# Optimization experiments

Measured on AMD Instinct MI355X. Metric: run time of the kernel, lower is better.

The kernel has to match this reference:

```python
import jax, jax.numpy as jnp
import numpy as np
from jax import lax

B, CIN, COUT, H, W = 4, 256, 256, 64, 64
K, DG, STRIDE, PAD, DIL = 3, 1, 1, 1, 1
K2 = K * K
CG = CIN // DG
HO = (H + 2 * PAD - DIL * (K - 1) - 1) // STRIDE + 1
WO = (W + 2 * PAD - DIL * (K - 1) - 1) // STRIDE + 1


def setup_inputs() -> dict:
    key = jax.random.key(0)
    k1, k2, k3 = jax.random.split(key, 3)
    inputs = jax.random.normal(k1, (B, CIN, H, W), jnp.float32)
    # original init_offset() zeros these; small random weights instead so offsets ~0.5px
    w_off = jax.random.normal(k2, (3 * DG * K2, CIN, K, K), jnp.float32) * 0.01
    b_off = jnp.zeros((3 * DG * K2,), jnp.float32)
    w_dcn = jax.random.normal(k3, (COUT, CIN, K, K), jnp.float32) * (1.0 / np.sqrt(CIN * K2))
    b_dcn = jnp.zeros((COUT,), jnp.float32)
    return {"inputs": inputs, "w_off": w_off, "b_off": b_off, "w_dcn": w_dcn, "b_dcn": b_dcn}


def _conv2d(x, w, b):
    y = lax.conv_general_dilated(x, w, (STRIDE, STRIDE), [(PAD, PAD), (PAD, PAD)],
                                 rhs_dilation=(DIL, DIL),
                                 dimension_numbers=("NCHW", "OIHW", "NCHW"))
    return y + b[None, :, None, None]


def _dcn_forward(inputs, w_off, b_off, w_dcn, b_dcn):
    # offset/mask branch (standard conv), then chunk into o1, o2, mask
    om = _conv2d(inputs, w_off, b_off)                      # [B, 3*DG*K2, HO, WO]
    o1, o2, m = jnp.split(om, 3, axis=1)
    offset = jnp.concatenate([o1, o2], axis=1)              # [B, 2*DG*K2, HO, WO]
    mask = jax.nn.sigmoid(m)                                # [B, DG*K2, HO, WO]

    # DCNv2 offset layout: per deformable group, K2 taps of (dy, dx)
    off = offset.reshape(B, DG, K2, 2, HO, WO)
    dy, dx = off[:, :, :, 0], off[:, :, :, 1]               # [B, DG, K2, HO, WO]

    taps = jnp.arange(K2)
    ki = (taps // K).astype(jnp.float32)
    kj = (taps % K).astype(jnp.float32)
    hb = (jnp.arange(HO, dtype=jnp.float32) * STRIDE - PAD)
    wb = (jnp.arange(WO, dtype=jnp.float32) * STRIDE - PAD)
    py = dy + hb[None, None, None, :, None] + (ki * DIL)[None, None, :, None, None]
    px = dx + wb[None, None, None, None, :] + (kj * DIL)[None, None, :, None, None]

    y0f, x0f = jnp.floor(py), jnp.floor(px)
    ly, lx = py - y0f, px - x0f
    y0, x0 = y0f.astype(jnp.int32), x0f.astype(jnp.int32)
    y1, x1 = y0 + 1, x0 + 1

    flat = inputs.reshape(B, DG, CG, H * W)

    def corner(yi, xi, wgt):
        valid = (yi >= 0) & (yi < H) & (xi >= 0) & (xi < W)
        yc = jnp.clip(yi, 0, H - 1)
        xc = jnp.clip(xi, 0, W - 1)
        idx = (yc * W + xc).reshape(B, DG, 1, K2 * HO * WO)
        idx = jnp.broadcast_to(idx, (B, DG, CG, K2 * HO * WO))
        v = jnp.take_along_axis(flat, idx, axis=3).reshape(B, DG, CG, K2, HO, WO)
        w = jnp.where(valid, wgt, 0.0)[:, :, None]          # zero outside (zero-pad bilinear)
        return v * w

    val = (corner(y0, x0, (1 - ly) * (1 - lx)) + corner(y0, x1, (1 - ly) * lx)
           + corner(y1, x0, ly * (1 - lx)) + corner(y1, x1, ly * lx))

    cols = val * mask.reshape(B, DG, 1, K2, HO, WO)         # modulated columns
    cols = cols.reshape(B, CIN * K2, HO * WO)
    out = jnp.einsum("ok,bkn->bon", w_dcn.reshape(COUT, CIN * K2), cols)
    out = out + b_dcn[None, :, None]
    return out.reshape(B, COUT, HO, WO)


def reference(inputs, w_off, b_off, w_dcn, b_dcn):
    return _dcn_forward(inputs, w_off, b_off, w_dcn, b_dcn)
```

## Files before the change

### kernel.cpp

```cpp
#include <hip/hip_runtime.h>
#include <hip/hip_bf16.h>

typedef __bf16 bf16x8 __attribute__((ext_vector_type(8)));
typedef __bf16 bf16x4 __attribute__((ext_vector_type(4)));
typedef float f32x4 __attribute__((ext_vector_type(4)));
typedef unsigned int u32x4 __attribute__((ext_vector_type(4)));

#define CIN 256
#define COUT 256
#define KDIM 2304

__device__ __forceinline__ void gload_lds16(const void* g, void* l) {
  __builtin_amdgcn_global_load_lds(
      (__attribute__((address_space(1))) unsigned int*)g,
      (__attribute__((address_space(3))) unsigned int*)l, 16, 0, 0);
}

__global__ __launch_bounds__(256) void k_prep_all(const float* __restrict__ wdcn,
                                                  const float* __restrict__ woff,
                                                  __bf16* __restrict__ Ag,
                                                  __bf16* __restrict__ Ah,
                                                  __bf16* __restrict__ Al) {
  int bid = blockIdx.x, tid = threadIdx.x;
  if (bid < 2304) {
    int t = bid * 256 + tid;
    int cout = t / KDIM;
    int r = t - cout * KDIM;
    int tap = r >> 8, cin = r & 255;
    Ag[t] = (__bf16)wdcn[(cout * 256 + cin) * 9 + tap];
  } else {
    int t = (bid - 2304) * 256 + tid;
    int j = t & 7;
    int l = (t >> 3) & 63;
    int mh = (t >> 9) & 1;
    int s = t >> 10;
    int tap = s >> 3, cc = s & 7;
    int ki = tap / 3, kj = tap - ki * 3;
    int oc = mh * 16 + (l & 15);
    int cin = cc * 32 + ((l >> 4) << 3) + j;
    float v = (oc < 27) ? woff[((oc * 256 + cin) * 3 + ki) * 3 + kj] : 0.f;
    __bf16 hi = (__bf16)v;
    __bf16 lo = (__bf16)(v - (float)hi);
    Ah[t] = hi;
    Al[t] = lo;
  }
}

__global__ __launch_bounds__(256) void k_tr(const float* __restrict__ in,
                                            __bf16* __restrict__ inT) {
  int h = blockIdx.x, b = blockIdx.y;
  int c = threadIdx.x;
  const float* src = in + ((((b << 8) + c) << 6) + h) * 64;
  __bf16* dst = inT + (((b << 12) + (h << 6)) << 8) + c;
#pragma unroll
  for (int w4 = 0; w4 < 16; ++w4) {
    f32x4 v = *(const f32x4*)(src + (w4 << 2));
#pragma unroll
    for (int k = 0; k < 4; ++k) dst[(((w4 << 2) + k)) << 8] = (__bf16)v[k];
  }
}

__global__ __launch_bounds__(256) void k_conv(const __bf16* __restrict__ inT,
                                              const __bf16* __restrict__ Ah,
                                              const __bf16* __restrict__ Al,
                                              float* __restrict__ omp) {
  __shared__ __bf16 xh[3 * 4 * 66 * 8];
  int tid = threadIdx.x;
  int l = tid & 63, wn = tid >> 6;
  int ho = blockIdx.x, b = blockIdx.y, ct = blockIdx.z;

  f32x4 acc[2];
  acc[0] = (f32x4){0.f, 0.f, 0.f, 0.f};
  acc[1] = (f32x4){0.f, 0.f, 0.f, 0.f};

  for (int chunk = 0; chunk < 4; ++chunk) {
    int cin0 = ct * 128 + chunk * 32;
    for (int i = tid; i < 792; i += 256) {
      int c = i % 66;
      int t2 = i / 66;
      int u = t2 & 3, r = t2 >> 2;
      int h = ho - 1 + r, w = c - 1;
      bool ok = ((unsigned)h < 64u) & ((unsigned)w < 64u);
      bf16x8 hv = (bf16x8){};
      if (ok)
        hv = *(const bf16x8*)(inT + ((((b << 12) + (h << 6) + w)) << 8) + cin0 +
                              (u << 3));
      *(bf16x8*)&xh[((r * 4 + u) * 66 + c) << 3] = hv;
    }
    __syncthreads();
    int scc = ct * 4 + chunk;
#pragma unroll
    for (int tap = 0; tap < 9; ++tap) {
      int s = tap * 8 + scc;
      int ki = tap / 3, kj = tap - ki * 3;
      bf16x8 ah0 = *(const bf16x8*)(Ah + (((s * 2 + 0) * 64 + l) << 3));
      bf16x8 ah1 = *(const bf16x8*)(Ah + (((s * 2 + 1) * 64 + l) << 3));
      bf16x8 al0 = *(const bf16x8*)(Al + (((s * 2 + 0) * 64 + l) << 3));
      bf16x8 al1 = *(const bf16x8*)(Al + (((s * 2 + 1) * 64 + l) << 3));
      int u = l >> 4;
      int sc = (wn << 4) + (l & 15) + kj;
      bf16x8 bh = *(const bf16x8*)&xh[((ki * 4 + u) * 66 + sc) << 3];
      acc[0] = __builtin_amdgcn_mfma_f32_16x16x32_bf16(ah0, bh, acc[0], 0, 0, 0);
      acc[1] = __builtin_amdgcn_mfma_f32_16x16x32_bf16(ah1, bh, acc[1], 0, 0, 0);
      acc[0] = __builtin_amdgcn_mfma_f32_16x16x32_bf16(al0, bh, acc[0], 0, 0, 0);
      acc[1] = __builtin_amdgcn_mfma_f32_16x16x32_bf16(al1, bh, acc[1], 0, 0, 0);
    }
    __syncthreads();
  }
  int n = (ho << 6) + (wn << 4) + (l & 15);
#pragma unroll
  for (int mh = 0; mh < 2; ++mh)
#pragma unroll
    for (int r = 0; r < 4; ++r) {
      int oc = mh * 16 + ((l >> 4) << 2) + r;
      if (oc < 27)
        omp[(((ct * 4 + b) * 27 + oc) << 12) + n] = acc[mh][r];
    }
}

__global__ __launch_bounds__(512, 4) void k_gemm(const __bf16* __restrict__ inT,
                                                 const float* __restrict__ omp,
                                                 const float* __restrict__ boff,
                                                 const __bf16* __restrict__ Ag,
                                                 const float* __restrict__ bdcn,
                                                 float* __restrict__ out) {
  __shared__ u32x4 sA[2048];
  __shared__ u32x4 sB[256];
  int tid = threadIdx.x;
  int l = tid & 63;
  int w = tid >> 6;
  int wm = w & 3, wh = w >> 2;
  int id = blockIdx.x;
  int x = id & 7, t = id >> 3;
  int b = x >> 1;
  int ntile = ((x & 1) << 6) + t;
  int sn = tid >> 4;
  int sc = tid & 15;
  int n_g = (ntile << 5) + sn;
  const __bf16* tb = inT + ((b << 12) << 8);

  f32x4 acc[4];
#pragma unroll
  for (int i = 0; i < 4; ++i) acc[i] = (f32x4){0.f, 0.f, 0.f, 0.f};

  float w00 = 0.f, w01 = 0.f, w10 = 0.f, w11 = 0.f;
  int o00 = 0, o01 = 0, o10 = 0, o11 = 0;

  for (int step = 0; step < 36; ++step) {
    int tap = step >> 2;
    int cin0 = (step & 3) << 6;
    if ((step & 3) == 0) {
      int ki = tap / 3, kj = tap - ki * 3;
      float dy = omp[((b * 27 + 2 * tap) << 12) + n_g] +
                 omp[(((4 + b) * 27 + 2 * tap) << 12) + n_g] + boff[2 * tap];
      float dx = omp[((b * 27 + 2 * tap + 1) << 12) + n_g] +
                 omp[(((4 + b) * 27 + 2 * tap + 1) << 12) + n_g] + boff[2 * tap + 1];
      float mv = omp[((b * 27 + 18 + tap) << 12) + n_g] +
                 omp[(((4 + b) * 27 + 18 + tap) << 12) + n_g] + boff[18 + tap];
      float msk = 1.f / (1.f + __expf(-mv));
      float py = dy + (float)((n_g >> 6) - 1 + ki);
      float px = dx + (float)((n_g & 63) - 1 + kj);
      float y0f = floorf(py), x0f = floorf(px);
      float ly = py - y0f, lx = px - x0f;
      int y0 = (int)y0f, x0 = (int)x0f;
      int y1 = y0 + 1, x1 = x0 + 1;
      bool vy0 = (y0 >= 0) & (y0 < 64), vy1 = (y1 >= 0) & (y1 < 64);
      bool vx0 = (x0 >= 0) & (x0 < 64), vx1 = (x1 >= 0) & (x1 < 64);
      float hy = 1.f - ly, hx = 1.f - lx;
      w00 = (vy0 & vx0) ? hy * hx * msk : 0.f;
      w01 = (vy0 & vx1) ? hy * lx * msk : 0.f;
      w10 = (vy1 & vx0) ? ly * hx * msk : 0.f;
      w11 = (vy1 & vx1) ? ly * lx * msk : 0.f;
      int y0c = min(max(y0, 0), 63), y1c = min(max(y1, 0), 63);
      int x0c = min(max(x0, 0), 63), x1c = min(max(x1, 0), 63);
      o00 = (y0c << 6) + x0c;
      o01 = (y0c << 6) + x1c;
      o10 = (y1c << 6) + x0c;
      o11 = (y1c << 6) + x1c;
    }
    int cb0 = cin0 + (sc << 2);
    bf16x4 cA = *(const bf16x4*)(tb + (o00 << 8) + cb0);
    bf16x4 cB = *(const bf16x4*)(tb + (o01 << 8) + cb0);
    bf16x4 cC = *(const bf16x4*)(tb + (o10 << 8) + cb0);
    bf16x4 cD = *(const bf16x4*)(tb + (o11 << 8) + cb0);
    bf16x4 vv;
#pragma unroll
    for (int j = 0; j < 4; ++j) {
      vv[j] = (__bf16)(w00 * (float)cA[j] + w01 * (float)cB[j] +
                       w10 * (float)cC[j] + w11 * (float)cD[j]);
    }
    __syncthreads();
    int kk0 = (tap << 8) + cin0;
#pragma unroll
    for (int i = 0; i < 4; ++i) {
      int slot = i * 512 + tid;
      int m = slot >> 3, j = slot & 7;
      int csrc = j ^ (m & 7);
      const __bf16* src = Ag + m * KDIM + kk0 + (csrc << 3);
      gload_lds16((const void*)src, (void*)&sA[i * 512 + (tid & ~63)]);
    }
    {
      unsigned long long* sB64 = (unsigned long long*)sB;
      int slot = (sn << 3) + ((sc >> 1) ^ (sn & 7));
      sB64[slot * 2 + (sc & 1)] = __builtin_bit_cast(unsigned long long, vv);
    }
    __syncthreads();
#pragma unroll
    for (int kt = 0; kt < 2; ++kt) {
      bf16x8 af[4], bfr;
      int cc = (kt << 2) + (l >> 4);
#pragma unroll
      for (int mf = 0; mf < 4; ++mf) {
        int m = (wm << 6) + (mf << 4) + (l & 15);
        af[mf] = __builtin_bit_cast(bf16x8, sA[(m << 3) + (cc ^ (m & 7))]);
      }
      {
        int n = (wh << 4) + (l & 15);
        bfr = __builtin_bit_cast(bf16x8, sB[(n << 3) + (cc ^ (n & 7))]);
      }
#pragma unroll
      for (int mf = 0; mf < 4; ++mf)
        acc[mf] = __builtin_amdgcn_mfma_f32_16x16x32_bf16(af[mf], bfr, acc[mf],
                                                          0, 0, 0);
    }
  }
#pragma unroll
  for (int mf = 0; mf < 4; ++mf)
#pragma unroll
    for (int r = 0; r < 4; ++r) {
      int m = (wm << 6) + (mf << 4) + ((l >> 4) << 2) + r;
      int n = (ntile << 5) + (wh << 4) + (l & 15);
      out[((b * COUT + m) << 12) + n] = acc[mf][r] + bdcn[m];
    }
}

extern "C" void kernel_launch(void* const* d_in, const int* in_sizes, int n_in,
                              void* d_out, int out_size, void* d_ws, size_t ws_size,
                              hipStream_t stream) {
  const float* in = (const float*)d_in[0];
  const float* woff = (const float*)d_in[1];
  const float* boff = (const float*)d_in[2];
  const float* wdcn = (const float*)d_in[3];
  const float* bdcn = (const float*)d_in[4];
  float* out = (float*)d_out;
  char* ws = (char*)d_ws;
  __bf16* Ag = (__bf16*)ws;
  __bf16* Ah = (__bf16*)(ws + 1179648);
  __bf16* Al = (__bf16*)(ws + 1327104);
  float* omp = (float*)(ws + 1474560);
  __bf16* inT = (__bf16*)(ws + 5013504);
  k_prep_all<<<2592, 256, 0, stream>>>(wdcn, woff, Ag, Ah, Al);
  k_tr<<<dim3(64, 4), 256, 0, stream>>>(in, inT);
  k_conv<<<dim3(64, 4, 2), 256, 0, stream>>>(inT, Ah, Al, omp);
  k_gemm<<<512, 512, 0, stream>>>(inT, omp, boff, Ag, bdcn, out);
}
```

Before: 93.27 us.

## Prefetch next-step bilinear gathers during MFMA and fuse transpose into prep kernel

The deformable GEMM kernel now issues the next step's offset/weight computation and four-corner gathers right after the LDS barrier, so those global loads are in flight while the current step's MFMAs run. Separately, the input transpose kernel is folded into the weight-prep kernel as extra blocks, removing one kernel launch. This costs extra registers to hold the prefetched corners, which may affect occupancy.

New measurement: 97.85 us. 1.05x slower.

```diff
diff --git a/kernel.cpp b/kernel.cpp
--- a/kernel.cpp
+++ b/kernel.cpp
@@ -18,9 +18,11 @@
 
 __global__ __launch_bounds__(256) void k_prep_all(const float* __restrict__ wdcn,
                                                   const float* __restrict__ woff,
+                                                  const float* __restrict__ in,
                                                   __bf16* __restrict__ Ag,
                                                   __bf16* __restrict__ Ah,
-                                                  __bf16* __restrict__ Al) {
+                                                  __bf16* __restrict__ Al,
+                                                  __bf16* __restrict__ inT) {
   int bid = blockIdx.x, tid = threadIdx.x;
   if (bid < 2304) {
     int t = bid * 256 + tid;
@@ -28,7 +30,7 @@
     int r = t - cout * KDIM;
     int tap = r >> 8, cin = r & 255;
     Ag[t] = (__bf16)wdcn[(cout * 256 + cin) * 9 + tap];
-  } else {
+  } else if (bid < 2592) {
     int t = (bid - 2304) * 256 + tid;
     int j = t & 7;
     int l = (t >> 3) & 63;
@@ -43,20 +45,18 @@
     __bf16 lo = (__bf16)(v - (float)hi);
     Ah[t] = hi;
     Al[t] = lo;
-  }
-}
-
-__global__ __launch_bounds__(256) void k_tr(const float* __restrict__ in,
-                                            __bf16* __restrict__ inT) {
-  int h = blockIdx.x, b = blockIdx.y;
-  int c = threadIdx.x;
-  const float* src = in + ((((b << 8) + c) << 6) + h) * 64;
-  __bf16* dst = inT + (((b << 12) + (h << 6)) << 8) + c;
-#pragma unroll
-  for (int w4 = 0; w4 < 16; ++w4) {
-    f32x4 v = *(const f32x4*)(src + (w4 << 2));
-#pragma unroll
-    for (int k = 0; k < 4; ++k) dst[(((w4 << 2) + k)) << 8] = (__bf16)v[k];
+  } else {
+    int idx = bid - 2592;
+    int h = idx & 63, b = idx >> 6;
+    int c = tid;
+    const float* src = in + ((((b << 8) + c) << 6) + h) * 64;
+    __bf16* dst = inT + (((b << 12) + (h << 6)) << 8) + c;
+#pragma unroll
+    for (int w4 = 0; w4 < 16; ++w4) {
+      f32x4 v = *(const f32x4*)(src + (w4 << 2));
+#pragma unroll
+      for (int k = 0; k < 4; ++k) dst[(((w4 << 2) + k)) << 8] = (__bf16)v[k];
+    }
   }
 }
 
@@ -145,44 +145,51 @@
 
   float w00 = 0.f, w01 = 0.f, w10 = 0.f, w11 = 0.f;
   int o00 = 0, o01 = 0, o10 = 0, o11 = 0;
+  bf16x4 cA, cB, cC, cD;
+
+  auto do_corners = [&](int tap) {
+    int ki = tap / 3, kj = tap - ki * 3;
+    float dy = omp[((b * 27 + 2 * tap) << 12) + n_g] +
+               omp[(((4 + b) * 27 + 2 * tap) << 12) + n_g] + boff[2 * tap];
+    float dx = omp[((b * 27 + 2 * tap + 1) << 12) + n_g] +
+               omp[(((4 + b) * 27 + 2 * tap + 1) << 12) + n_g] + boff[2 * tap + 1];
+    float mv = omp[((b * 27 + 18 + tap) << 12) + n_g] +
+               omp[(((4 + b) * 27 + 18 + tap) << 12) + n_g] + boff[18 + tap];
+    float msk = 1.f / (1.f + __expf(-mv));
+    float py = dy + (float)((n_g >> 6) - 1 + ki);
+    float px = dx + (float)((n_g & 63) - 1 + kj);
+    float y0f = floorf(py), x0f = floorf(px);
+    float ly = py - y0f, lx = px - x0f;
+    int y0 = (int)y0f, x0 = (int)x0f;
+    int y1 = y0 + 1, x1 = x0 + 1;
+    bool vy0 = (y0 >= 0) & (y0 < 64), vy1 = (y1 >= 0) & (y1 < 64);
+    bool vx0 = (x0 >= 0) & (x0 < 64), vx1 = (x1 >= 0) & (x1 < 64);
+    float hy = 1.f - ly, hx = 1.f - lx;
+    w00 = (vy0 & vx0) ? hy * hx * msk : 0.f;
+    w01 = (vy0 & vx1) ? hy * lx * msk : 0.f;
+    w10 = (vy1 & vx0) ? ly * hx * msk : 0.f;
+    w11 = (vy1 & vx1) ? ly * lx * msk : 0.f;
+    int y0c = min(max(y0, 0), 63), y1c = min(max(y1, 0), 63);
+    int x0c = min(max(x0, 0), 63), x1c = min(max(x1, 0), 63);
+    o00 = (y0c << 6) + x0c;
+    o01 = (y0c << 6) + x1c;
+    o10 = (y1c << 6) + x0c;
+    o11 = (y1c << 6) + x1c;
+  };
+  auto do_gather = [&](int s1) {
+    int cb0 = ((s1 & 3) << 6) + (sc << 2);
+    cA = *(const bf16x4*)(tb + (o00 << 8) + cb0);
+    cB = *(const bf16x4*)(tb + (o01 << 8) + cb0);
+    cC = *(const bf16x4*)(tb + (o10 << 8) + cb0);
+    cD = *(const bf16x4*)(tb + (o11 << 8) + cb0);
+  };
+
+  do_corners(0);
+  do_gather(0);
 
   for (int step = 0; step < 36; ++step) {
     int tap = step >> 2;
     int cin0 = (step & 3) << 6;
-    if ((step & 3) == 0) {
-      int ki = tap / 3, kj = tap - ki * 3;
-      float dy = omp[((b * 27 + 2 * tap) << 12) + n_g] +
-                 omp[(((4 + b) * 27 + 2 * tap) << 12) + n_g] + boff[2 * tap];
-      float dx = omp[((b * 27 + 2 * tap + 1) << 12) + n_g] +
-                 omp[(((4 + b) * 27 + 2 * tap + 1) << 12) + n_g] + boff[2 * tap + 1];
-      float mv = omp[((b * 27 + 18 + tap) << 12) + n_g] +
-                 omp[(((4 + b) * 27 + 18 + tap) << 12) + n_g] + boff[18 + tap];
-      float msk = 1.f / (1.f + __expf(-mv));
-      float py = dy + (float)((n_g >> 6) - 1 + ki);
-      float px = dx + (float)((n_g & 63) - 1 + kj);
-      float y0f = floorf(py), x0f = floorf(px);
-      float ly = py - y0f, lx = px - x0f;
-      int y0 = (int)y0f, x0 = (int)x0f;
-      int y1 = y0 + 1, x1 = x0 + 1;
-      bool vy0 = (y0 >= 0) & (y0 < 64), vy1 = (y1 >= 0) & (y1 < 64);
-      bool vx0 = (x0 >= 0) & (x0 < 64), vx1 = (x1 >= 0) & (x1 < 64);
-      float hy = 1.f - ly, hx = 1.f - lx;
-      w00 = (vy0 & vx0) ? hy * hx * msk : 0.f;
-      w01 = (vy0 & vx1) ? hy * lx * msk : 0.f;
-      w10 = (vy1 & vx0) ? ly * hx * msk : 0.f;
-      w11 = (vy1 & vx1) ? ly * lx * msk : 0.f;
-      int y0c = min(max(y0, 0), 63), y1c = min(max(y1, 0), 63);
-      int x0c = min(max(x0, 0), 63), x1c = min(max(x1, 0), 63);
-      o00 = (y0c << 6) + x0c;
-      o01 = (y0c << 6) + x1c;
-      o10 = (y1c << 6) + x0c;
-      o11 = (y1c << 6) + x1c;
-    }
-    int cb0 = cin0 + (sc << 2);
-    bf16x4 cA = *(const bf16x4*)(tb + (o00 << 8) + cb0);
-    bf16x4 cB = *(const bf16x4*)(tb + (o01 << 8) + cb0);
-    bf16x4 cC = *(const bf16x4*)(tb + (o10 << 8) + cb0);
-    bf16x4 cD = *(const bf16x4*)(tb + (o11 << 8) + cb0);
     bf16x4 vv;
 #pragma unroll
     for (int j = 0; j < 4; ++j) {
@@ -205,6 +212,11 @@
       sB64[slot * 2 + (sc & 1)] = __builtin_bit_cast(unsigned long long, vv);
     }
     __syncthreads();
+    if (step < 35) {
+      int s1 = step + 1;
+      if ((s1 & 3) == 0) do_corners(s1 >> 2);
+      do_gather(s1);
+    }
 #pragma unroll
     for (int kt = 0; kt < 2; ++kt) {
       bf16x8 af[4], bfr;
@@ -249,8 +261,7 @@
   __bf16* Al = (__bf16*)(ws + 1327104);
   float* omp = (float*)(ws + 1474560);
   __bf16* inT = (__bf16*)(ws + 5013504);
-  k_prep_all<<<2592, 256, 0, stream>>>(wdcn, woff, Ag, Ah, Al);
-  k_tr<<<dim3(64, 4), 256, 0, stream>>>(in, inT);
+  k_prep_all<<<2848, 256, 0, stream>>>(wdcn, woff, in, Ag, Ah, Al, inT);
   k_conv<<<dim3(64, 4, 2), 256, 0, stream>>>(inT, Ah, Al, omp);
   k_gemm<<<512, 512, 0, stream>>>(inT, omp, boff, Ag, bdcn, out);
 }
```

## Merge input transpose into prep kernel, vectorize prep writes, stage conv weights in LDS

Applied to the files above, without the earlier changes.

Folds the input transpose kernel into the weight-prep kernel, removing one launch. The prep threads now write eight bf16 values at a time instead of one. The offset-conv kernel copies each chunk's hi/lo weight slices into shared memory with global_load_lds and reads MFMA operands from LDS instead of global memory. This cuts launch overhead and redundant global weight loads, at the cost of 36KB more LDS per block, which may lower occupancy.

Result: faster. 82.68 us (-11.3%).

```diff
diff --git a/kernel.cpp b/kernel.cpp
--- a/kernel.cpp
+++ b/kernel.cpp
@@ -18,45 +18,54 @@
 
 __global__ __launch_bounds__(256) void k_prep_all(const float* __restrict__ wdcn,
                                                   const float* __restrict__ woff,
+                                                  const float* __restrict__ in,
                                                   __bf16* __restrict__ Ag,
                                                   __bf16* __restrict__ Ah,
-                                                  __bf16* __restrict__ Al) {
+                                                  __bf16* __restrict__ Al,
+                                                  __bf16* __restrict__ inT) {
   int bid = blockIdx.x, tid = threadIdx.x;
-  if (bid < 2304) {
-    int t = bid * 256 + tid;
-    int cout = t / KDIM;
-    int r = t - cout * KDIM;
-    int tap = r >> 8, cin = r & 255;
-    Ag[t] = (__bf16)wdcn[(cout * 256 + cin) * 9 + tap];
-  } else {
-    int t = (bid - 2304) * 256 + tid;
-    int j = t & 7;
-    int l = (t >> 3) & 63;
-    int mh = (t >> 9) & 1;
-    int s = t >> 10;
+  if (bid < 288) {
+    int t8 = bid * 256 + tid;
+    int cout = t8 / 288;
+    int r8 = t8 - cout * 288;
+    int tap = r8 >> 5;
+    int cin0 = (r8 & 31) << 3;
+    bf16x8 vv;
+#pragma unroll
+    for (int j = 0; j < 8; ++j)
+      vv[j] = (__bf16)wdcn[(cout * 256 + cin0 + j) * 9 + tap];
+    *(bf16x8*)&Ag[t8 << 3] = vv;
+  } else if (bid < 324) {
+    int t8 = (bid - 288) * 256 + tid;
+    int l = t8 & 63;
+    int mh = (t8 >> 6) & 1;
+    int s = t8 >> 7;
     int tap = s >> 3, cc = s & 7;
     int ki = tap / 3, kj = tap - ki * 3;
     int oc = mh * 16 + (l & 15);
-    int cin = cc * 32 + ((l >> 4) << 3) + j;
-    float v = (oc < 27) ? woff[((oc * 256 + cin) * 3 + ki) * 3 + kj] : 0.f;
-    __bf16 hi = (__bf16)v;
-    __bf16 lo = (__bf16)(v - (float)hi);
-    Ah[t] = hi;
-    Al[t] = lo;
-  }
-}
-
-__global__ __launch_bounds__(256) void k_tr(const float* __restrict__ in,
-                                            __bf16* __restrict__ inT) {
-  int h = blockIdx.x, b = blockIdx.y;
-  int c = threadIdx.x;
-  const float* src = in + ((((b << 8) + c) << 6) + h) * 64;
-  __bf16* dst = inT + (((b << 12) + (h << 6)) << 8) + c;
-#pragma unroll
-  for (int w4 = 0; w4 < 16; ++w4) {
-    f32x4 v = *(const f32x4*)(src + (w4 << 2));
-#pragma unroll
-    for (int k = 0; k < 4; ++k) dst[(((w4 << 2) + k)) << 8] = (__bf16)v[k];
+    int cinb = cc * 32 + ((l >> 4) << 3);
+    bf16x8 hv, lv;
+#pragma unroll
+    for (int j = 0; j < 8; ++j) {
+      float v = (oc < 27) ? woff[((oc * 256 + cinb + j) * 3 + ki) * 3 + kj] : 0.f;
+      __bf16 hi = (__bf16)v;
+      hv[j] = hi;
+      lv[j] = (__bf16)(v - (float)hi);
+    }
+    *(bf16x8*)&Ah[t8 << 3] = hv;
+    *(bf16x8*)&Al[t8 << 3] = lv;
+  } else {
+    int idx = bid - 324;
+    int h = idx & 63, b = idx >> 6;
+    int c = tid;
+    const float* src = in + ((((b << 8) + c) << 6) + h) * 64;
+    __bf16* dst = inT + (((b << 12) + (h << 6)) << 8) + c;
+#pragma unroll
+    for (int w4 = 0; w4 < 16; ++w4) {
+      f32x4 v = *(const f32x4*)(src + (w4 << 2));
+#pragma unroll
+      for (int k = 0; k < 4; ++k) dst[(((w4 << 2) + k)) << 8] = (__bf16)v[k];
+    }
   }
 }
 
@@ -65,6 +74,7 @@
                                               const __bf16* __restrict__ Al,
                                               float* __restrict__ omp) {
   __shared__ __bf16 xh[3 * 4 * 66 * 8];
+  __shared__ __bf16 sW[2 * 9 * 1024];
   int tid = threadIdx.x;
   int l = tid & 63, wn = tid >> 6;
   int ho = blockIdx.x, b = blockIdx.y, ct = blockIdx.z;
@@ -75,6 +85,18 @@
 
   for (int chunk = 0; chunk < 4; ++chunk) {
     int cin0 = ct * 128 + chunk * 32;
+    int scc = ct * 4 + chunk;
+    u32x4* sW4 = (u32x4*)sW;
+#pragma unroll
+    for (int i = 0; i < 9; ++i) {
+      int s = i * 256 + tid;
+      int a = s / 1152;
+      int r = s - a * 1152;
+      int tap = r >> 7, w = r & 127;
+      const __bf16* src =
+          (a ? Al : Ah) + (((tap * 8 + scc) * 2) << 9) + (w << 3);
+      gload_lds16((const void*)src, (void*)&sW4[i * 256 + (tid & ~63)]);
+    }
     for (int i = tid; i < 792; i += 256) {
       int c = i % 66;
       int t2 = i / 66;
@@ -88,15 +110,13 @@
       *(bf16x8*)&xh[((r * 4 + u) * 66 + c) << 3] = hv;
     }
     __syncthreads();
-    int scc = ct * 4 + chunk;
 #pragma unroll
     for (int tap = 0; tap < 9; ++tap) {
-      int s = tap * 8 + scc;
       int ki = tap / 3, kj = tap - ki * 3;
-      bf16x8 ah0 = *(const bf16x8*)(Ah + (((s * 2 + 0) * 64 + l) << 3));
-      bf16x8 ah1 = *(const bf16x8*)(Ah + (((s * 2 + 1) * 64 + l) << 3));
-      bf16x8 al0 = *(const bf16x8*)(Al + (((s * 2 + 0) * 64 + l) << 3));
-      bf16x8 al1 = *(const bf16x8*)(Al + (((s * 2 + 1) * 64 + l) << 3));
+      bf16x8 ah0 = *(const bf16x8*)&sW[tap * 1024 + (l << 3)];
+      bf16x8 ah1 = *(const bf16x8*)&sW[tap * 1024 + 512 + (l << 3)];
+      bf16x8 al0 = *(const bf16x8*)&sW[9216 + tap * 1024 + (l << 3)];
+      bf16x8 al1 = *(const bf16x8*)&sW[9216 + tap * 1024 + 512 + (l << 3)];
       int u = l >> 4;
       int sc = (wn << 4) + (l & 15) + kj;
       bf16x8 bh = *(const bf16x8*)&xh[((ki * 4 + u) * 66 + sc) << 3];
@@ -249,8 +269,7 @@
   __bf16* Al = (__bf16*)(ws + 1327104);
   float* omp = (float*)(ws + 1474560);
   __bf16* inT = (__bf16*)(ws + 5013504);
-  k_prep_all<<<2592, 256, 0, stream>>>(wdcn, woff, Ag, Ah, Al);
-  k_tr<<<dim3(64, 4), 256, 0, stream>>>(in, inT);
+  k_prep_all<<<580, 256, 0, stream>>>(wdcn, woff, in, Ag, Ah, Al, inT);
   k_conv<<<dim3(64, 4, 2), 256, 0, stream>>>(inT, Ah, Al, omp);
   k_gemm<<<512, 512, 0, stream>>>(inT, omp, boff, Ag, bdcn, out);
 }
```
